# Optimization experiments

Measured on AMD Instinct MI355X. Metric: run time of the kernel, lower is better.

The kernel has to match this reference:

```python
import jax, jax.numpy as jnp
import numpy as np

IOU_TH = 0.5      # iou_threshold
SCORE_TH = 0.5    # confidence_threshold (passed as score_threshold to tf NMS)
MAX_DET = 512     # max_detections


def setup_inputs() -> dict:
    key = jax.random.key(0)
    k1, k2, k3 = jax.random.split(key, 3)
    B, N, C = 8, 2048, 80
    # tf.image.non_max_suppression interprets box columns as corners
    # (y1, x1, y2, x2); generate valid corner boxes in [0, 1].
    mins = jax.random.uniform(k1, (B, N, 2), dtype=jnp.float32)
    sizes = jax.random.uniform(k2, (B, N, 2), dtype=jnp.float32) * 0.2 + 0.01
    box_prediction = jnp.concatenate([mins, mins + sizes], axis=-1)  # [B,N,4]
    class_prediction = jax.random.normal(k3, (B, N, C), dtype=jnp.float32) * 2.0
    return {"box_prediction": box_prediction, "class_prediction": class_prediction}


def _nms_single(boxes, cls_pred, conf):
    """Greedy NMS for one image. boxes [N,4], cls_pred [N,C], conf [N].
    Matches tf.image.non_max_suppression semantics (corner-coordinate IoU,
    score threshold, greedy suppression in descending score order),
    then gathers boxes/cls/conf at the kept indices, padded to MAX_DET."""
    N = boxes.shape[0]
    order = jnp.argsort(-conf)                 # descending scores
    b = boxes[order]                            # [N,4]
    c = cls_pred[order]                         # [N,C]
    s = conf[order]                             # [N]

    bb = jax.lax.stop_gradient(b)               # IoU/indices are non-diff
    y1, x1, y2, x2 = bb[:, 0], bb[:, 1], bb[:, 2], bb[:, 3]
    area = (y2 - y1) * (x2 - x1)                # [N]
    ih = jnp.clip(jnp.minimum(y2[:, None], y2[None, :]) -
                  jnp.maximum(y1[:, None], y1[None, :]), 0.0)
    iw = jnp.clip(jnp.minimum(x2[:, None], x2[None, :]) -
                  jnp.maximum(x1[:, None], x1[None, :]), 0.0)
    inter = ih * iw                             # [N,N]
    union = area[:, None] + area[None, :] - inter
    iou = inter / jnp.maximum(union, 1e-9)      # [N,N]

    valid = s > SCORE_TH                        # score_threshold filter
    idxs = jnp.arange(N)

    def step(keep, xs):
        row, i = xs
        # if box i survives, suppress all later boxes overlapping > IOU_TH
        sup = (row > IOU_TH) & (idxs > i) & keep[i]
        return keep & ~sup, None

    keep, _ = jax.lax.scan(step, valid, (iou, idxs))

    # select kept boxes (already sorted by score) padded to MAX_DET
    masked = jnp.where(keep, s, -1.0)
    top_s, top_idx = jax.lax.top_k(jax.lax.stop_gradient(masked), MAX_DET)
    vm = top_s > SCORE_TH                       # validity of each output slot
    out_box = b[top_idx] * vm[:, None].astype(b.dtype)
    out_cls = c[top_idx] * vm[:, None].astype(c.dtype)
    out_conf = jnp.where(vm, s[top_idx], 0.0)
    return out_box, out_cls, out_conf


def reference(box_prediction, class_prediction):
    # from_logits=True branch of the layer
    class_confidence = jnp.max(jax.nn.sigmoid(class_prediction), axis=-1)  # [B,N]
    cls_prob = jax.nn.softmax(class_prediction, axis=-1)                   # [B,N,C]
    nms_box, nms_cls, nms_conf = jax.vmap(_nms_single)(
        box_prediction, cls_prob, class_confidence)
    return nms_box, nms_cls, nms_conf
```

## Files before the change

### kernel.cpp

```cpp
#include <hip/hip_runtime.h>
#include <stdint.h>

#define BB 8
#define NN 2048
#define NC 80
#define MAXDET 512
#define WPR 32


#define ORD_HALF 0xBF000000u

__global__ void k_conf(const float* __restrict__ cls, uint64_t* __restrict__ keys) {
    int gid = blockIdx.x * blockDim.x + threadIdx.x;
    const float4* p = (const float4*)(cls + (size_t)gid * NC);
    float m = -3.0e38f;
#pragma unroll
    for (int i = 0; i < NC / 4; ++i) {
        float4 v = p[i];
        m = fmaxf(m, fmaxf(fmaxf(v.x, v.y), fmaxf(v.z, v.w)));
    }
    float e  = expf(-m);
    float cf = 1.0f / (1.0f + e);
    uint32_t u = __float_as_uint(cf);
    u = (u & 0x80000000u) ? ~u : (u | 0x80000000u);
    int n = gid & (NN - 1);
    keys[gid] = ((uint64_t)u << 32) | (uint32_t)(NN - 1 - n);
}

#define RCHUNK 128
__global__ __launch_bounds__(512) void k_rank(const uint64_t* __restrict__ keys_in,
                                              uint64_t* __restrict__ keys_out,
                                              const float* __restrict__ boxes,
                                              float* __restrict__ sboxes) {
    __shared__ uint64_t sk[NN];
    __shared__ uint16_t part[4][RCHUNK];
    int b = blockIdx.y, t = threadIdx.x;
    const uint64_t* kin = keys_in + (size_t)b * NN;
#pragma unroll
    for (int j = 0; j < NN / 512; ++j)
        sk[t + j * 512] = kin[t + j * 512];
    __syncthreads();
    int sub = t >> 7;
    int el  = t & (RCHUNK - 1);
    int e   = blockIdx.x * RCHUNK + el;
    uint64_t mykey = sk[e];
    int base = sub * (NN / 4);
    int r = 0;
    for (int mm = 0; mm < NN / 4; ++mm)
        r += (sk[base + mm] > mykey) ? 1 : 0;
    part[sub][el] = (uint16_t)r;
    __syncthreads();
    if (t < RCHUNK) {
        int rank = part[0][t] + part[1][t] + part[2][t] + part[3][t];
        keys_out[(size_t)b * NN + rank] = mykey;
        int orig = (NN - 1) - (int)(mykey & 0xFFFFFFFFull);
        ((float4*)sboxes)[(size_t)b * NN + rank] =
            ((const float4*)boxes)[(size_t)b * NN + orig];
    }
}

__global__ void k_sup(const float* __restrict__ sboxes, uint64_t* __restrict__ sup) {
#pragma clang fp contract(off)
    __shared__ float cy1[256], cx1[256], cy2[256], cx2[256], car[256];
    __shared__ float ry1[64], rx1[64], ry2[64], rx2[64], rar[64];
    int rt = blockIdx.x, ct = blockIdx.y, b = blockIdx.z;
    int t = threadIdx.x;
    int col0 = ct << 8, row0 = rt << 6;
    {
        float4 bx = ((const float4*)sboxes)[(size_t)b * NN + col0 + t];
        cy1[t] = bx.x; cx1[t] = bx.y; cy2[t] = bx.z; cx2[t] = bx.w;
        car[t] = (bx.z - bx.x) * (bx.w - bx.y);
        if (t < 64) {
            float4 rb = ((const float4*)sboxes)[(size_t)b * NN + row0 + t];
            ry1[t] = rb.x; rx1[t] = rb.y; ry2[t] = rb.z; rx2[t] = rb.w;
            rar[t] = (rb.z - rb.x) * (rb.w - rb.y);
        }
    }
    __syncthreads();
    int lr = t & 63, lg = t >> 6;
    int r = row0 + lr;
    int gw = (ct << 2) + lg;
    int cbase = gw << 6;
    uint64_t w = 0;
    if (cbase + 63 > r) {
        float y1 = ry1[lr], x1 = rx1[lr], y2 = ry2[lr], x2 = rx2[lr], ar = rar[lr];
        int lcb = lg << 6;
        for (int c = 0; c < 64; ++c) {
            int lc = lcb + c;
            float ih = fmaxf(fminf(y2, cy2[lc]) - fmaxf(y1, cy1[lc]), 0.0f);
            float iw = fmaxf(fminf(x2, cx2[lc]) - fmaxf(x1, cx1[lc]), 0.0f);
            float inter = ih * iw;
            float uni = (ar + car[lc]) - inter;
            float iou = inter / fmaxf(uni, 1e-9f);
            if ((iou > 0.5f) & ((cbase + c) > r)) w |= (1ull << c);
        }
    }
    sup[((size_t)b * NN + r) * WPR + gw] = w;
}

#define NMS_THREADS 320
__global__ __launch_bounds__(NMS_THREADS) void k_nms(const uint64_t* __restrict__ keys,
                                                     const float* __restrict__ sboxes,
                                                     const uint64_t* __restrict__ sup,
                                                     int* __restrict__ kidx,
                                                     int* __restrict__ kcount,
                                                     float* __restrict__ out_box,
                                                     float* __restrict__ out_conf) {
    __shared__ uint64_t buf[2][64 * WPR];
    __shared__ uint8_t  val[NN];
    __shared__ uint64_t kmaskS[WPR];
    __shared__ int pfx[WPR];
    __shared__ int s_kc;
    __shared__ int s_done;
    int b = blockIdx.x, t = threadIdx.x;
    const uint64_t* supb = sup + (size_t)b * NN * WPR;
    const uint64_t* keyb = keys + (size_t)b * NN;

    for (int i = t; i < NN; i += NMS_THREADS)
        val[i] = (uint8_t)((uint32_t)(keyb[i] >> 32) > ORD_HALF);
    if (t < WPR) kmaskS[t] = 0;
    if (t == 0) s_done = 0;
    for (int w = t; w < 64 * WPR / 2; w += NMS_THREADS)
        ((float4*)buf[0])[w] = ((const float4*)supb)[w];
    __syncthreads();

    int wave = t >> 6;
    uint64_t kb = 0;
    int cnt = 0;
    if (t < 32) {
        uint64_t vm = 0;
#pragma unroll
        for (int c = 0; c < 64; ++c)
            vm |= ((uint64_t)val[(t << 6) | c]) << c;
        kb = ~vm;
    }

    for (int g = 0; g < WPR; ++g) {
        if (wave > 0) {
            if (g + 1 < WPR) {
                const float4* src = (const float4*)(supb + (size_t)(g + 1) * 64 * WPR);
                float4* dst = (float4*)buf[(g + 1) & 1];
                int idx = t - 64;
                float4 r0 = src[idx];
                float4 r1 = src[idx + 256];
                float4 r2 = src[idx + 512];
                float4 r3 = src[idx + 768];
                dst[idx]       = r0;
                dst[idx + 256] = r1;
                dst[idx + 512] = r2;
                dst[idx + 768] = r3;
            }
        } else if (t < 32) {
            const int l = t;
            const uint64_t* bufc = buf[g & 1];
            uint64_t rw = __shfl(kb, g);
            uint64_t gm = 0;
#pragma unroll
            for (int c = 0; c < 64; ++c) {
                uint64_t rowg = bufc[c * WPR + g];
                uint64_t rowl = bufc[c * WPR + l];
                bool kept = (((rw >> c) & 1ull) == 0);
                if (kept) {
                    rw |= rowg;
                    kb |= rowl;
                    gm |= (1ull << c);
                }
            }
            if (l == g) kmaskS[g] = gm;
            cnt += __popcll(gm);
            if (cnt >= MAXDET) s_done = 1;
        }
        __syncthreads();
        if (s_done) break;
    }

    if (t == 0) {
        int s = 0;
        for (int w2 = 0; w2 < WPR; ++w2) { pfx[w2] = s; s += __popcll(kmaskS[w2]); }
        s_kc = (s < MAXDET) ? s : MAXDET;
        kcount[b] = s_kc;
    }
    __syncthreads();
    for (int i = t; i < NN; i += NMS_THREADS) {
        uint64_t m = kmaskS[i >> 6];
        if ((m >> (i & 63)) & 1ull) {
            int rank = pfx[i >> 6] + __popcll(m & ((1ull << (i & 63)) - 1ull));
            if (rank < MAXDET) {
                ((float4*)out_box)[(size_t)b * MAXDET + rank] =
                    ((const float4*)sboxes)[(size_t)b * NN + i];
                uint64_t kk = keyb[i];
                uint32_t u = (uint32_t)(kk >> 32);
                float cf = (u & 0x80000000u) ? __uint_as_float(u ^ 0x80000000u)
                                             : __uint_as_float(~u);
                out_conf[(size_t)b * MAXDET + rank] = cf;
                kidx[b * MAXDET + rank] = (NN - 1) - (int)(kk & 0xFFFFFFFFull);
            }
        }
    }
    for (int k = s_kc + t; k < MAXDET; k += NMS_THREADS) {
        ((float4*)out_box)[(size_t)b * MAXDET + k] = make_float4(0.f, 0.f, 0.f, 0.f);
        out_conf[(size_t)b * MAXDET + k] = 0.0f;
    }
}

__global__ void k_softmax(const float* __restrict__ cls, const int* __restrict__ kidx,
                          const int* __restrict__ kcount, float* __restrict__ out_cls) {
    int k = blockIdx.x, b = blockIdx.y, lane = threadIdx.x;
    float* dst = out_cls + ((size_t)b * MAXDET + k) * NC;
    if (k >= kcount[b]) {
        dst[lane] = 0.0f;
        if (lane < NC - 64) dst[64 + lane] = 0.0f;
        return;
    }
    int n = kidx[b * MAXDET + k];
    const float* src = cls + ((size_t)b * NN + n) * NC;
    float x0 = src[lane];
    float x1 = (lane < NC - 64) ? src[64 + lane] : -3.0e38f;
    float m = fmaxf(x0, x1);
    for (int o = 32; o > 0; o >>= 1) m = fmaxf(m, __shfl_xor(m, o));
    float e0 = expf(x0 - m);
    float e1 = (lane < NC - 64) ? expf(x1 - m) : 0.0f;
    float s = e0 + e1;
    for (int o = 32; o > 0; o >>= 1) s += __shfl_xor(s, o);
    dst[lane] = e0 / s;
    if (lane < NC - 64) dst[64 + lane] = e1 / s;
}

extern "C" void kernel_launch(void* const* d_in, const int* in_sizes, int n_in,
                              void* d_out, int out_size, void* d_ws, size_t ws_size,
                              hipStream_t stream) {
    const float* boxes = (const float*)d_in[0];
    const float* cls   = (const float*)d_in[1];
    float* out      = (float*)d_out;
    float* out_box  = out;
    float* out_cls  = out + BB * MAXDET * 4;
    float* out_conf = out + BB * MAXDET * (4 + NC);

    char* ws = (char*)d_ws;
    uint64_t* keysA  = (uint64_t*)(ws + 0);
    uint64_t* keysB  = (uint64_t*)(ws + 131072);
    float*    sboxes = (float*)(ws + 262144);
    int*      kidx   = (int*)(ws + 524288);
    int*      kcount = (int*)(ws + 540672);
    uint64_t* sup    = (uint64_t*)(ws + 544768);

    k_conf<<<(BB * NN) / 256, 256, 0, stream>>>(cls, keysA);
    k_rank<<<dim3(NN / RCHUNK, BB), 512, 0, stream>>>(keysA, keysB, boxes, sboxes);
    k_sup<<<dim3(NN / 64, NN / 256, BB), 256, 0, stream>>>(sboxes, sup);
    k_nms<<<BB, NMS_THREADS, 0, stream>>>(keysB, sboxes, sup, kidx, kcount, out_box, out_conf);
    k_softmax<<<dim3(MAXDET, BB), 64, 0, stream>>>(cls, kidx, kcount, out_cls);
}
```

Measured before the change: 88.82 us.

## Resolve NMS diagonal block with scalar readlane chain and split row OR across full wave

The serial greedy pass inside each 64-box group now loads the diagonal block into lanes and walks it with readlane on scalar registers, so the dependent chain no longer waits on a shared-memory load per step. The later OR of kept rows into each lane's keep mask is done separately by all 64 lanes of wave 0, each half of the wave covering 32 candidate rows, then combined with a shuffle. The aim is to shorten the latency-bound critical path of the sequential suppression loop. In exchange the wave does more instructions per group and uses more lanes.

```diff
diff --git a/kernel.cpp b/kernel.cpp
--- a/kernel.cpp
+++ b/kernel.cpp
@@ -134,6 +134,7 @@
             vm |= ((uint64_t)val[(t << 6) | c]) << c;
         kb = ~vm;
     }
+    int l2 = t & 31, half = (t >> 5) & 1;
 
     for (int g = 0; g < WPR; ++g) {
         if (wave > 0) {
@@ -150,23 +151,42 @@
                 dst[idx + 512] = r2;
                 dst[idx + 768] = r3;
             }
-        } else if (t < 32) {
-            const int l = t;
+        } else {
             const uint64_t* bufc = buf[g & 1];
-            uint64_t rw = __shfl(kb, g);
-            uint64_t gm = 0;
-#pragma unroll
-            for (int c = 0; c < 64; ++c) {
-                uint64_t rowg = bufc[c * WPR + g];
-                uint64_t rowl = bufc[c * WPR + l];
-                bool kept = (((rw >> c) & 1ull) == 0);
-                if (kept) {
-                    rw |= rowg;
-                    kb |= rowl;
-                    gm |= (1ull << c);
+            uint64_t diag = bufc[t * WPR + g];
+            uint32_t dlo = (uint32_t)diag, dhi = (uint32_t)(diag >> 32);
+            uint64_t rwv = __shfl(kb, g);
+            uint32_t rw_lo = __builtin_amdgcn_readfirstlane((uint32_t)rwv);
+            uint32_t rw_hi = __builtin_amdgcn_readfirstlane((uint32_t)(rwv >> 32));
+            uint32_t gm_lo = 0, gm_hi = 0;
+#pragma unroll
+            for (int c = 0; c < 32; ++c) {
+                uint32_t rlo = __builtin_amdgcn_readlane(dlo, c);
+                uint32_t rhi = __builtin_amdgcn_readlane(dhi, c);
+                if (((rw_lo >> c) & 1u) == 0u) {
+                    rw_lo |= rlo; rw_hi |= rhi; gm_lo |= (1u << c);
                 }
             }
-            if (l == g) kmaskS[g] = gm;
+#pragma unroll
+            for (int c = 0; c < 32; ++c) {
+                uint32_t rlo = __builtin_amdgcn_readlane(dlo, c + 32);
+                uint32_t rhi = __builtin_amdgcn_readlane(dhi, c + 32);
+                if (((rw_hi >> c) & 1u) == 0u) {
+                    rw_lo |= rlo; rw_hi |= rhi; gm_hi |= (1u << c);
+                }
+            }
+            uint64_t gm = ((uint64_t)gm_hi << 32) | gm_lo;
+            uint32_t gmh = half ? gm_hi : gm_lo;
+            const uint64_t* rowp = bufc + ((half << 5) * WPR + l2);
+            uint64_t acc = 0;
+#pragma unroll
+            for (int j = 0; j < 32; ++j) {
+                uint64_t row = rowp[(size_t)j * WPR];
+                if ((gmh >> j) & 1u) acc |= row;
+            }
+            acc |= __shfl(acc, t ^ 32);
+            if (t < 32) kb |= acc;
+            if (t == g) kmaskS[g] = gm;
             cnt += __popcll(gm);
             if (cnt >= MAXDET) s_done = 1;
         }
```

Measured after the change: 85.56 us. -3.7%, faster.
